# Optimization experiments

Measured on AMD Instinct MI355X. Metric: run time of the kernel, lower is better.

## Reference

```python
import jax, jax.numpy as jnp
import numpy as np

B, S, H = 2, 1024, 4096
NH, NKV, HD = 32, 8, 128
GROUPS = NH // NKV  # num_key_value_groups
ROPE_THETA = 10000.0


def setup_inputs() -> dict:
    key = jax.random.key(0)
    k0, k1, k2 = jax.random.split(key, 3)
    x = jax.random.normal(k0, (B, S, H), jnp.float32)
    w_qkv = jax.random.normal(k1, (H, (NH + 2 * NKV) * HD), jnp.float32) * (1.0 / np.sqrt(H))
    w_o = jax.random.normal(k2, (NH * HD, H), jnp.float32) * (1.0 / np.sqrt(H))
    # rotary cos/sin tables (llama freqs_cis, interleaved-pair convention)
    inv_freq = 1.0 / (ROPE_THETA ** (np.arange(0, HD, 2, dtype=np.float64) / HD))
    freqs = np.outer(np.arange(S, dtype=np.float64), inv_freq)  # [S, HD/2]
    cos = jnp.asarray(np.cos(freqs), jnp.float32)
    sin = jnp.asarray(np.sin(freqs), jnp.float32)
    # additive causal mask [1,1,S,S]
    causal = np.tril(np.ones((S, S), dtype=bool))
    mask = jnp.asarray(np.where(causal, 0.0, -1e9), jnp.float32)[None, None]
    return {"x": x, "w_qkv": w_qkv, "w_o": w_o, "cos": cos, "sin": sin, "mask": mask}


def _rope(t, cos, sin):
    # t: [B,S,N,HD]; rotate interleaved (even, odd) pairs like complex mult by freqs_cis
    t2 = t.reshape(t.shape[:-1] + (HD // 2, 2))
    t0, t1 = t2[..., 0], t2[..., 1]
    c = cos[None, :, None, :]  # [1,S,1,HD/2]
    s = sin[None, :, None, :]
    r0 = t0 * c - t1 * s
    r1 = t0 * s + t1 * c
    return jnp.stack([r0, r1], axis=-1).reshape(t.shape)


def reference(x, w_qkv, w_o, cos, sin, mask):
    b, s, _ = x.shape
    xqkv = (x @ w_qkv).reshape(b, s, NH + 2 * NKV, HD)
    xq = xqkv[:, :, :NH]                  # [b,s,NH,HD]
    xk = xqkv[:, :, NH:NH + NKV]          # [b,s,NKV,HD]
    xv = xqkv[:, :, NH + NKV:]            # [b,s,NKV,HD]
    xq = _rope(xq, cos, sin)
    xk = _rope(xk, cos, sin)
    # GQA: repeat kv heads to match query heads (repeat_interleave on head dim)
    k = jnp.repeat(xk, GROUPS, axis=2)
    v = jnp.repeat(xv, GROUPS, axis=2)
    scores = jnp.einsum('bqhd,bkhd->bhqk', xq, k) / np.float32(np.sqrt(HD))
    scores = scores + mask
    probs = jax.nn.softmax(scores.astype(jnp.float32), axis=-1).astype(xq.dtype)
    out = jnp.einsum('bhqk,bkhd->bqhd', probs, v).reshape(b, s, NH * HD)
    return out @ w_o
```

## Files before the change

### kernel.cpp

```cpp
#include <hip/hip_runtime.h>
#include <cstdint>
#include <cstddef>

typedef short bf16x8 __attribute__((ext_vector_type(8)));
typedef float f32x4 __attribute__((ext_vector_type(4)));

__device__ __forceinline__ unsigned short f2bf(float f) {
  unsigned int u = __builtin_bit_cast(unsigned int, f);
  u += 0x7fffu + ((u >> 16) & 1u);
  return (unsigned short)(u >> 16);
}

__global__ void k_convert(const float* __restrict__ in, unsigned short* __restrict__ out, int n4) {
  int i = blockIdx.x * blockDim.x + threadIdx.x;
  if (i >= n4) return;
  float4 v = ((const float4*)in)[i];
  ushort4 o;
  o.x = f2bf(v.x); o.y = f2bf(v.y); o.z = f2bf(v.z); o.w = f2bf(v.w);
  ((ushort4*)out)[i] = o;
}

__global__ __launch_bounds__(256) void k_transpose(const float* __restrict__ src,
                                                   unsigned short* __restrict__ dst,
                                                   int K, int N) {
  __shared__ float t[64][65];
  const int n0 = blockIdx.x * 64, k0 = blockIdx.y * 64;
  const int tid = threadIdx.x;
  const int lr = tid >> 4, lc = (tid & 15) * 4;
#pragma unroll
  for (int i = 0; i < 4; ++i) {
    float4 v = *(const float4*)(src + (size_t)(k0 + i * 16 + lr) * N + n0 + lc);
    t[i * 16 + lr][lc] = v.x;
    t[i * 16 + lr][lc + 1] = v.y;
    t[i * 16 + lr][lc + 2] = v.z;
    t[i * 16 + lr][lc + 3] = v.w;
  }
  __syncthreads();
  const int nr = tid >> 3, kk = (tid & 7) * 8;
#pragma unroll
  for (int i = 0; i < 2; ++i) {
    int n = nr + i * 32;
    bf16x8 v;
#pragma unroll
    for (int j = 0; j < 8; ++j) v[j] = (short)f2bf(t[kk + j][n]);
    *(bf16x8*)(dst + (size_t)(n0 + n) * K + k0 + kk) = v;
  }
}

template <int MODE>
__global__ __launch_bounds__(256) void k_gemm(const unsigned short* __restrict__ A,
                                              const unsigned short* __restrict__ Bt,
                                              float* __restrict__ C,
                                              unsigned short* __restrict__ Qr,
                                              unsigned short* __restrict__ Kr,
                                              unsigned short* __restrict__ Vt,
                                              const float* __restrict__ cosT,
                                              const float* __restrict__ sinT,
                                              int M, int N, int K) {
  __shared__ __align__(16) unsigned short lA[128 * 64];
  __shared__ __align__(16) unsigned short lB[128 * 64];
  const int tid = threadIdx.x;
  const int lane = tid & 63, wv = tid >> 6;
  const int wr = wv >> 1, wc = wv & 1;
  const int lid = blockIdx.y * gridDim.x + blockIdx.x;
  const int cpx = (gridDim.x * gridDim.y) >> 3;
  const int swz = (lid & 7) * cpx + (lid >> 3);
  const int bm = (swz % gridDim.x) * 128, bn = (swz / gridDim.x) * 128;
  const int l16 = lane & 15, lhi = lane >> 4;
  f32x4 acc[4][4] = {};
  bf16x8 ar[4], br[4];

#pragma unroll
  for (int i = 0; i < 4; ++i) {
    int c = tid + i * 256, row = c >> 3, c16 = c & 7;
    ar[i] = *(const bf16x8*)(A + (size_t)(bm + row) * K + 0 + c16 * 8);
    br[i] = *(const bf16x8*)(Bt + (size_t)(bn + row) * K + 0 + c16 * 8);
  }
  const int nkt = K >> 6;
  for (int kt = 0; kt < nkt; ++kt) {
    __syncthreads();
#pragma unroll
    for (int i = 0; i < 4; ++i) {
      int c = tid + i * 256, row = c >> 3, c16 = c & 7;
      int pc = c16 ^ (row & 7);
      *(bf16x8*)((char*)lA + row * 128 + pc * 16) = ar[i];
      *(bf16x8*)((char*)lB + row * 128 + pc * 16) = br[i];
    }
    __syncthreads();
    if (kt + 1 < nkt) {
      int kofs = (kt + 1) << 6;
#pragma unroll
      for (int i = 0; i < 4; ++i) {
        int c = tid + i * 256, row = c >> 3, c16 = c & 7;
        ar[i] = *(const bf16x8*)(A + (size_t)(bm + row) * K + kofs + c16 * 8);
        br[i] = *(const bf16x8*)(Bt + (size_t)(bn + row) * K + kofs + c16 * 8);
      }
    }
#pragma unroll
    for (int s = 0; s < 2; ++s) {
      bf16x8 af[4], bfr[4];
#pragma unroll
      for (int f = 0; f < 4; ++f) {
        int rowa = wr * 64 + f * 16 + l16;
        int ca = (s * 4 + lhi) ^ (rowa & 7);
        af[f] = *(const bf16x8*)((char*)lA + rowa * 128 + ca * 16);
        int rowb = wc * 64 + f * 16 + l16;
        int cb = (s * 4 + lhi) ^ (rowb & 7);
        bfr[f] = *(const bf16x8*)((char*)lB + rowb * 128 + cb * 16);
      }
#pragma unroll
      for (int fi = 0; fi < 4; ++fi)
#pragma unroll
        for (int fj = 0; fj < 4; ++fj)
          acc[fi][fj] = __builtin_amdgcn_mfma_f32_16x16x32_bf16(af[fi], bfr[fj], acc[fi][fj], 0, 0, 0);
    }
  }

  if (MODE == 0) {
#pragma unroll
    for (int fi = 0; fi < 4; ++fi) {
      int rbase = bm + wr * 64 + fi * 16 + lhi * 4;
#pragma unroll
      for (int fj = 0; fj < 4; ++fj) {
        int col = bn + wc * 64 + fj * 16 + l16;
#pragma unroll
        for (int r = 0; r < 4; ++r)
          C[(size_t)(rbase + r) * N + col] = acc[fi][fj][r];
      }
    }
  } else {
#pragma unroll
    for (int fi = 0; fi < 4; ++fi) {
      int rbase = bm + wr * 64 + fi * 16 + lhi * 4;
      int b = rbase >> 10, sbase = rbase & 1023;
#pragma unroll
      for (int fj = 0; fj < 4; ++fj) {
        int col = bn + wc * 64 + fj * 16 + l16;
        if (col < 5120) {
          int i = (col & 127) >> 1;
          float sgn = (col & 1) ? 1.0f : -1.0f;
          unsigned short* dst;
          if (col < 4096)
            dst = Qr + ((size_t)(b * 32 + (col >> 7)) * 1024) * 128 + (col & 127);
          else
            dst = Kr + ((size_t)(b * 8 + ((col - 4096) >> 7)) * 1024) * 128 + (col & 127);
#pragma unroll
          for (int r = 0; r < 4; ++r) {
            float own = acc[fi][fj][r];
            float other = __shfl_xor(own, 1);
            int s = sbase + r;
            float c = cosT[s * 64 + i], sn = sinT[s * 64 + i];
            dst[(size_t)s * 128] = f2bf(own * c + sgn * other * sn);
          }
        } else {
          int kvh = (col - 5120) >> 7, d = col & 127;
          unsigned short* dst = Vt + ((size_t)(b * 8 + kvh) * 128 + d) * 1024;
#pragma unroll
          for (int r = 0; r < 4; ++r) dst[sbase + r] = f2bf(acc[fi][fj][r]);
        }
      }
    }
  }
}

__global__ __launch_bounds__(256) void k_attn(const unsigned short* __restrict__ Qr,
                                              const unsigned short* __restrict__ Kr,
                                              const unsigned short* __restrict__ Vt,
                                              unsigned short* __restrict__ Out) {
  __shared__ __align__(16) unsigned short lK[64 * 128];
  __shared__ __align__(16) unsigned short lV[128 * 64];
  __shared__ __align__(16) unsigned short lP[4 * 16 * 64];
  const int tid = threadIdx.x, lane = tid & 63, wv = tid >> 6;
  const int qt = blockIdx.x, h = blockIdx.y, b = blockIdx.z;
  const int kvh = h >> 2;
  const int q0 = qt * 64;
  const int l16 = lane & 15, lhi = lane >> 4;

  const unsigned short* Qbase = Qr + ((size_t)(b * 32 + h) * 1024 + q0 + wv * 16 + l16) * 128;
  bf16x8 qf[4];
#pragma unroll
  for (int s = 0; s < 4; ++s) qf[s] = *(const bf16x8*)(Qbase + s * 32 + lhi * 8);

  const unsigned short* Kbase = Kr + (size_t)(b * 8 + kvh) * 1024 * 128;
  const unsigned short* Vbase = Vt + (size_t)(b * 8 + kvh) * 128 * 1024;

  f32x4 oacc[8] = {};
  float mrow[4] = {-1e30f, -1e30f, -1e30f, -1e30f};
  float lrow[4] = {0.f, 0.f, 0.f, 0.f};
  const int ntk = qt + 1;
  bf16x8 kreg[4], vreg[4];

#pragma unroll
  for (int i = 0; i < 4; ++i) {
    int c = tid + i * 256;
    int krow = c >> 4, kc = c & 15;
    kreg[i] = *(const bf16x8*)(Kbase + (size_t)krow * 128 + kc * 8);
    int vrow = c >> 3, vc = c & 7;
    vreg[i] = *(const bf16x8*)(Vbase + (size_t)vrow * 1024 + vc * 8);
  }

  for (int kt = 0; kt < ntk; ++kt) {
    const int k0 = kt * 64;
    __syncthreads();
#pragma unroll
    for (int i = 0; i < 4; ++i) {
      int c = tid + i * 256;
      int krow = c >> 4, kc = c & 15;
      *(bf16x8*)((char*)lK + krow * 256 + (kc ^ (krow & 7)) * 16) = kreg[i];
      int vrow = c >> 3, vc = c & 7;
      *(bf16x8*)((char*)lV + vrow * 128 + (vc ^ (vrow & 7)) * 16) = vreg[i];
    }
    __syncthreads();

    if (kt + 1 < ntk) {
      const int kn = (kt + 1) * 64;
#pragma unroll
      for (int i = 0; i < 4; ++i) {
        int c = tid + i * 256;
        int krow = c >> 4, kc = c & 15;
        kreg[i] = *(const bf16x8*)(Kbase + (size_t)(kn + krow) * 128 + kc * 8);
        int vrow = c >> 3, vc = c & 7;
        vreg[i] = *(const bf16x8*)(Vbase + (size_t)vrow * 1024 + kn + vc * 8);
      }
    }

    f32x4 sacc[4] = {};
#pragma unroll
    for (int kf = 0; kf < 4; ++kf) {
      int rowk = kf * 16 + l16;
#pragma unroll
      for (int s = 0; s < 4; ++s) {
        int ck = (s * 4 + lhi) ^ (rowk & 7);
        bf16x8 kfr = *(const bf16x8*)((char*)lK + rowk * 256 + ck * 16);
        sacc[kf] = __builtin_amdgcn_mfma_f32_16x16x32_bf16(qf[s], kfr, sacc[kf], 0, 0, 0);
      }
    }

    const int qg = q0 + wv * 16 + lhi * 4;
    float mt[4] = {-1e30f, -1e30f, -1e30f, -1e30f};
#pragma unroll
    for (int kf = 0; kf < 4; ++kf) {
      int kg = k0 + kf * 16 + l16;
#pragma unroll
      for (int r = 0; r < 4; ++r) {
        float v = sacc[kf][r] * 0.08838834764831845f;
        v = (kg <= qg + r) ? v : -1e9f;
        sacc[kf][r] = v;
        mt[r] = fmaxf(mt[r], v);
      }
    }
#pragma unroll
    for (int r = 0; r < 4; ++r) {
#pragma unroll
      for (int off = 1; off < 16; off <<= 1) mt[r] = fmaxf(mt[r], __shfl_xor(mt[r], off));
    }
    float alpha[4], rs[4];
#pragma unroll
    for (int r = 0; r < 4; ++r) {
      float mn = fmaxf(mrow[r], mt[r]);
      alpha[r] = __expf(mrow[r] - mn);
      mrow[r] = mn;
      rs[r] = 0.f;
    }
#pragma unroll
    for (int kf = 0; kf < 4; ++kf) {
      int key = kf * 16 + l16;
#pragma unroll
      for (int r = 0; r < 4; ++r) {
        float p = __expf(sacc[kf][r] - mrow[r]);
        rs[r] += p;
        int prow = lhi * 4 + r;
        int addr = wv * 2048 + ((prow * 128 + key * 2) ^ ((prow & 7) << 4));
        *(unsigned short*)((char*)lP + addr) = f2bf(p);
      }
    }
#pragma unroll
    for (int r = 0; r < 4; ++r) {
#pragma unroll
      for (int off = 1; off < 16; off <<= 1) rs[r] += __shfl_xor(rs[r], off);
      lrow[r] = lrow[r] * alpha[r] + rs[r];
    }
#pragma unroll
    for (int nf = 0; nf < 8; ++nf)
#pragma unroll
      for (int r = 0; r < 4; ++r) oacc[nf][r] *= alpha[r];

#pragma unroll
    for (int s2 = 0; s2 < 2; ++s2) {
      int prow = l16;
      int paddr = wv * 2048 + ((prow * 128 + s2 * 64 + lhi * 16) ^ ((prow & 7) << 4));
      bf16x8 pa = *(const bf16x8*)((char*)lP + paddr);
#pragma unroll
      for (int nf = 0; nf < 8; ++nf) {
        int rowd = nf * 16 + l16;
        int cv = (s2 * 4 + lhi) ^ (rowd & 7);
        bf16x8 vfr = *(const bf16x8*)((char*)lV + rowd * 128 + cv * 16);
        oacc[nf] = __builtin_amdgcn_mfma_f32_16x16x32_bf16(pa, vfr, oacc[nf], 0, 0, 0);
      }
    }
  }

  unsigned short* Ob = Out + ((size_t)(b * 1024) + q0 + wv * 16 + lhi * 4) * 4096 + h * 128;
#pragma unroll
  for (int r = 0; r < 4; ++r) {
    float inv = 1.f / lrow[r];
#pragma unroll
    for (int nf = 0; nf < 8; ++nf)
      Ob[(size_t)r * 4096 + nf * 16 + l16] = f2bf(oacc[nf][r] * inv);
  }
}

extern "C" void kernel_launch(void* const* d_in, const int* in_sizes, int n_in,
                              void* d_out, int out_size, void* d_ws, size_t ws_size,
                              hipStream_t stream) {
  const float* x = (const float*)d_in[0];
  const float* w_qkv = (const float*)d_in[1];
  const float* w_o = (const float*)d_in[2];
  const float* cosT = (const float*)d_in[3];
  const float* sinT = (const float*)d_in[4];

  char* ws = (char*)d_ws;
  unsigned short* wqkv_t = (unsigned short*)(ws);
  unsigned short* wo_t   = (unsigned short*)(ws + 50331648);
  unsigned short* xb     = (unsigned short*)(ws + 83886080);
  unsigned short* Qr     = (unsigned short*)(ws + 100663296);
  unsigned short* Kr     = (unsigned short*)(ws + 117440512);
  unsigned short* Vt     = (unsigned short*)(ws + 121634816);
  unsigned short* attn   = (unsigned short*)(ws + 125829120);

  k_convert<<<8192, 256, 0, stream>>>(x, xb, 2048 * 4096 / 4);
  k_transpose<<<dim3(6144 / 64, 4096 / 64), 256, 0, stream>>>(w_qkv, wqkv_t, 4096, 6144);
  k_transpose<<<dim3(4096 / 64, 4096 / 64), 256, 0, stream>>>(w_o, wo_t, 4096, 4096);
  k_gemm<1><<<dim3(16, 48), 256, 0, stream>>>(xb, wqkv_t, nullptr, Qr, Kr, Vt, cosT, sinT,
                                              2048, 6144, 4096);
  k_attn<<<dim3(16, 32, 2), 256, 0, stream>>>(Qr, Kr, Vt, attn);
  k_gemm<0><<<dim3(16, 32), 256, 0, stream>>>(attn, wo_t, (float*)d_out, nullptr, nullptr, nullptr,
                                              nullptr, nullptr, 2048, 4096, 4096);
}
```

Baseline: 329.2 us.

## Replace QKV GEMM with 256x256 tiled 8-phase pipelined kernel using direct-to-LDS loads

Adds a new QKV projection GEMM with 256x256 output tiles, 512 threads and a double-buffered LDS. Tiles are staged with global_load_lds direct-to-LDS copies, interleaved across eight compute phases with explicit vmcnt waits, barriers and setprio. The goal is more data reuse per tile and overlap of global loads with MFMA work, in place of the 128x128 register-staged GEMM. The fused RoPE/V-transpose epilogue is kept, and the output GEMM becomes a non-template kernel. This adds hand-tuned waitcnt logic that must line up exactly with the load counts, and the 192-block grid may leave some compute units idle.

```diff
diff --git a/kernel.cpp b/kernel.cpp
--- a/kernel.cpp
+++ b/kernel.cpp
@@ -9,6 +9,12 @@
   unsigned int u = __builtin_bit_cast(unsigned int, f);
   u += 0x7fffu + ((u >> 16) & 1u);
   return (unsigned short)(u >> 16);
+}
+
+__device__ __forceinline__ void gload_lds(const unsigned short* g, unsigned short* l) {
+  __builtin_amdgcn_global_load_lds(
+      (const __attribute__((address_space(1))) unsigned int*)g,
+      (__attribute__((address_space(3))) unsigned int*)l, 16, 0, 0);
 }
 
 __global__ void k_convert(const float* __restrict__ in, unsigned short* __restrict__ out, int n4) {
@@ -47,16 +53,131 @@
   }
 }
 
-template <int MODE>
+__global__ __launch_bounds__(512, 2) void k_gemm8p(const unsigned short* __restrict__ A,
+                                                   const unsigned short* __restrict__ Bt,
+                                                   unsigned short* __restrict__ Qr,
+                                                   unsigned short* __restrict__ Kr,
+                                                   unsigned short* __restrict__ Vt,
+                                                   const float* __restrict__ cosT,
+                                                   const float* __restrict__ sinT) {
+  __shared__ __align__(16) unsigned short lds[2][2][2][128 * 64];
+  const int tid = threadIdx.x;
+  const int lane = tid & 63, wv = tid >> 6;
+  const int wr = wv >> 2, wc = wv & 3;
+  const int l16 = lane & 15, lhi = lane >> 4;
+  const int lid = blockIdx.x;
+  const int swz = (lid & 7) * 24 + (lid >> 3);
+  const int bm2 = (swz & 7) * 256, bn2 = (swz >> 3) * 256;
+
+  f32x4 acc[8][4] = {};
+
+  auto STAGE = [&](int buf, int mat, int half, const unsigned short* srcM, int srcRowBase, int kt) {
+#pragma unroll
+    for (int j = 0; j < 2; ++j) {
+      int row = j * 64 + wv * 8 + (lane >> 3);
+      int chunk = (lane & 7) ^ (row & 7);
+      gload_lds(srcM + (size_t)(srcRowBase + row) * 4096 + kt * 64 + chunk * 8,
+                &lds[buf][mat][half][(j * 512 + wv * 64) * 8]);
+    }
+  };
+
+  auto PHASE = [&](int buf, int mh, int nh, int stg, int b2, int m2, int h2,
+                   const unsigned short* s2, int rb2, int kt2, int vm) {
+    bf16x8 af[4][2], bfr[2][2];
+#pragma unroll
+    for (int fl = 0; fl < 4; ++fl) {
+      int ra = fl * 32 + wr * 16 + l16;
+#pragma unroll
+      for (int s = 0; s < 2; ++s)
+        af[fl][s] = *(const bf16x8*)&lds[buf][0][mh][ra * 64 + (((s * 4 + lhi) ^ (ra & 7)) * 8)];
+    }
+#pragma unroll
+    for (int fl = 0; fl < 2; ++fl) {
+      int rb = fl * 64 + wc * 16 + l16;
+#pragma unroll
+      for (int s = 0; s < 2; ++s)
+        bfr[fl][s] = *(const bf16x8*)&lds[buf][1][nh][rb * 64 + (((s * 4 + lhi) ^ (rb & 7)) * 8)];
+    }
+    if (stg) STAGE(b2, m2, h2, s2, rb2, kt2);
+    __builtin_amdgcn_s_barrier();
+    __builtin_amdgcn_s_setprio(1);
+#pragma unroll
+    for (int fl = 0; fl < 4; ++fl)
+#pragma unroll
+      for (int gl = 0; gl < 2; ++gl)
+#pragma unroll
+        for (int s = 0; s < 2; ++s)
+          acc[mh * 4 + fl][nh * 2 + gl] =
+              __builtin_amdgcn_mfma_f32_16x16x32_bf16(af[fl][s], bfr[gl][s],
+                                                      acc[mh * 4 + fl][nh * 2 + gl], 0, 0, 0);
+    __builtin_amdgcn_s_setprio(0);
+    if (vm == 4) {
+      asm volatile("s_waitcnt vmcnt(4)" ::: "memory");
+      __builtin_amdgcn_sched_barrier(0);
+    } else if (vm == 0) {
+      asm volatile("s_waitcnt vmcnt(0)" ::: "memory");
+      __builtin_amdgcn_sched_barrier(0);
+    }
+    __builtin_amdgcn_s_barrier();
+  };
+
+  STAGE(0, 0, 0, A, bm2, 0);       STAGE(0, 0, 1, A, bm2 + 128, 0);
+  STAGE(0, 1, 0, Bt, bn2, 0);      STAGE(0, 1, 1, Bt, bn2 + 128, 0);
+  STAGE(1, 0, 0, A, bm2, 1);       STAGE(1, 0, 1, A, bm2 + 128, 1);
+  STAGE(1, 1, 0, Bt, bn2, 1);      STAGE(1, 1, 1, Bt, bn2 + 128, 1);
+  asm volatile("s_waitcnt vmcnt(8)" ::: "memory");
+  __builtin_amdgcn_sched_barrier(0);
+  __builtin_amdgcn_s_barrier();
+
+  for (int i = 0; i < 32; ++i) {
+    const int t1 = 2 * i + 1, t2 = 2 * i + 2, t3 = 2 * i + 3;
+    const int nf = (i > 0), nl = (i < 31);
+    PHASE(0, 0, 0, nf, 1, 0, 0, A, bm2, t1, -1);
+    PHASE(0, 1, 0, nf, 1, 1, 1, Bt, bn2 + 128, t1, -1);
+    PHASE(0, 1, 1, nl, 0, 1, 0, Bt, bn2, t2, -1);
+    PHASE(0, 0, 1, nl, 0, 0, 1, A, bm2 + 128, t2, nl ? 4 : 0);
+    PHASE(1, 0, 0, nl, 0, 0, 0, A, bm2, t2, -1);
+    PHASE(1, 1, 0, nl, 0, 1, 1, Bt, bn2 + 128, t2, -1);
+    PHASE(1, 1, 1, nl, 1, 1, 0, Bt, bn2, t3, -1);
+    PHASE(1, 0, 1, nl, 1, 0, 1, A, bm2 + 128, t3, nl ? 4 : -1);
+  }
+
+#pragma unroll
+  for (int fi = 0; fi < 8; ++fi) {
+    int rbase = bm2 + fi * 32 + wr * 16 + lhi * 4;
+    int b = rbase >> 10, sbase = rbase & 1023;
+#pragma unroll
+    for (int fj = 0; fj < 4; ++fj) {
+      int col = bn2 + fj * 64 + wc * 16 + l16;
+      if (col < 5120) {
+        int ip = (col & 127) >> 1;
+        float sgn = (col & 1) ? 1.0f : -1.0f;
+        unsigned short* dst;
+        if (col < 4096)
+          dst = Qr + ((size_t)(b * 32 + (col >> 7)) * 1024) * 128 + (col & 127);
+        else
+          dst = Kr + ((size_t)(b * 8 + ((col - 4096) >> 7)) * 1024) * 128 + (col & 127);
+#pragma unroll
+        for (int r = 0; r < 4; ++r) {
+          float own = acc[fi][fj][r];
+          float other = __shfl_xor(own, 1);
+          int s = sbase + r;
+          float c = cosT[s * 64 + ip], sn = sinT[s * 64 + ip];
+          dst[(size_t)s * 128] = f2bf(own * c + sgn * other * sn);
+        }
+      } else {
+        int kvh = (col - 5120) >> 7, d = col & 127;
+        unsigned short* dst = Vt + ((size_t)(b * 8 + kvh) * 128 + d) * 1024;
+#pragma unroll
+        for (int r = 0; r < 4; ++r) dst[sbase + r] = f2bf(acc[fi][fj][r]);
+      }
+    }
+  }
+}
+
 __global__ __launch_bounds__(256) void k_gemm(const unsigned short* __restrict__ A,
                                               const unsigned short* __restrict__ Bt,
-                                              float* __restrict__ C,
-                                              unsigned short* __restrict__ Qr,
-                                              unsigned short* __restrict__ Kr,
-                                              unsigned short* __restrict__ Vt,
-                                              const float* __restrict__ cosT,
-                                              const float* __restrict__ sinT,
-                                              int M, int N, int K) {
+                                              float* __restrict__ C, int M, int N, int K) {
   __shared__ __align__(16) unsigned short lA[128 * 64];
   __shared__ __align__(16) unsigned short lB[128 * 64];
   const int tid = threadIdx.x;
@@ -115,50 +236,15 @@
           acc[fi][fj] = __builtin_amdgcn_mfma_f32_16x16x32_bf16(af[fi], bfr[fj], acc[fi][fj], 0, 0, 0);
     }
   }
-
-  if (MODE == 0) {
-#pragma unroll
-    for (int fi = 0; fi < 4; ++fi) {
-      int rbase = bm + wr * 64 + fi * 16 + lhi * 4;
-#pragma unroll
-      for (int fj = 0; fj < 4; ++fj) {
-        int col = bn + wc * 64 + fj * 16 + l16;
-#pragma unroll
-        for (int r = 0; r < 4; ++r)
-          C[(size_t)(rbase + r) * N + col] = acc[fi][fj][r];
-      }
-    }
-  } else {
-#pragma unroll
-    for (int fi = 0; fi < 4; ++fi) {
-      int rbase = bm + wr * 64 + fi * 16 + lhi * 4;
-      int b = rbase >> 10, sbase = rbase & 1023;
-#pragma unroll
-      for (int fj = 0; fj < 4; ++fj) {
-        int col = bn + wc * 64 + fj * 16 + l16;
-        if (col < 5120) {
-          int i = (col & 127) >> 1;
-          float sgn = (col & 1) ? 1.0f : -1.0f;
-          unsigned short* dst;
-          if (col < 4096)
-            dst = Qr + ((size_t)(b * 32 + (col >> 7)) * 1024) * 128 + (col & 127);
-          else
-            dst = Kr + ((size_t)(b * 8 + ((col - 4096) >> 7)) * 1024) * 128 + (col & 127);
-#pragma unroll
-          for (int r = 0; r < 4; ++r) {
-            float own = acc[fi][fj][r];
-            float other = __shfl_xor(own, 1);
-            int s = sbase + r;
-            float c = cosT[s * 64 + i], sn = sinT[s * 64 + i];
-            dst[(size_t)s * 128] = f2bf(own * c + sgn * other * sn);
-          }
-        } else {
-          int kvh = (col - 5120) >> 7, d = col & 127;
-          unsigned short* dst = Vt + ((size_t)(b * 8 + kvh) * 128 + d) * 1024;
-#pragma unroll
-          for (int r = 0; r < 4; ++r) dst[sbase + r] = f2bf(acc[fi][fj][r]);
-        }
-      }
+#pragma unroll
+  for (int fi = 0; fi < 4; ++fi) {
+    int rbase = bm + wr * 64 + fi * 16 + lhi * 4;
+#pragma unroll
+    for (int fj = 0; fj < 4; ++fj) {
+      int col = bn + wc * 64 + fj * 16 + l16;
+#pragma unroll
+      for (int r = 0; r < 4; ++r)
+        C[(size_t)(rbase + r) * N + col] = acc[fi][fj][r];
     }
   }
 }
@@ -331,9 +417,7 @@
   k_convert<<<8192, 256, 0, stream>>>(x, xb, 2048 * 4096 / 4);
   k_transpose<<<dim3(6144 / 64, 4096 / 64), 256, 0, stream>>>(w_qkv, wqkv_t, 4096, 6144);
   k_transpose<<<dim3(4096 / 64, 4096 / 64), 256, 0, stream>>>(w_o, wo_t, 4096, 4096);
-  k_gemm<1><<<dim3(16, 48), 256, 0, stream>>>(xb, wqkv_t, nullptr, Qr, Kr, Vt, cosT, sinT,
-                                              2048, 6144, 4096);
+  k_gemm8p<<<192, 512, 0, stream>>>(xb, wqkv_t, Qr, Kr, Vt, cosT, sinT);
   k_attn<<<dim3(16, 32, 2), 256, 0, stream>>>(Qr, Kr, Vt, attn);
-  k_gemm<0><<<dim3(16, 32), 256, 0, stream>>>(attn, wo_t, (float*)d_out, nullptr, nullptr, nullptr,
-                                              nullptr, nullptr, 2048, 4096, 4096);
-}
+  k_gemm<<<dim3(16, 32), 256, 0, stream>>>(attn, wo_t, (float*)d_out, 2048, 4096, 4096);
+}
```

Measured after the change: 347.8 us. +5.7%, slower.

## Double attention query tile per block and merge prep kernels into one launch

Applied to the files above, without the earlier changes.

The attention kernel now handles 128 queries per block, with each wave covering two 16-row query groups. Each K/V tile loaded into LDS therefore feeds twice as many MFMAs, which halves K/V global traffic and staging per query. The cost is more registers (launch bounds set to 2 blocks per SIMD), half as many blocks, and more causal-diagonal waste since the last two key tiles are partly masked. Separately, the bf16 conversion of x and the two weight transposes are fused into one launch to remove launch overhead.

```diff
diff --git a/kernel.cpp b/kernel.cpp
--- a/kernel.cpp
+++ b/kernel.cpp
@@ -11,21 +11,10 @@
   return (unsigned short)(u >> 16);
 }
 
-__global__ void k_convert(const float* __restrict__ in, unsigned short* __restrict__ out, int n4) {
-  int i = blockIdx.x * blockDim.x + threadIdx.x;
-  if (i >= n4) return;
-  float4 v = ((const float4*)in)[i];
-  ushort4 o;
-  o.x = f2bf(v.x); o.y = f2bf(v.y); o.z = f2bf(v.z); o.w = f2bf(v.w);
-  ((ushort4*)out)[i] = o;
-}
-
-__global__ __launch_bounds__(256) void k_transpose(const float* __restrict__ src,
-                                                   unsigned short* __restrict__ dst,
-                                                   int K, int N) {
+__device__ __forceinline__ void transpose_tile(const float* __restrict__ src,
+                                               unsigned short* __restrict__ dst,
+                                               int K, int N, int n0, int k0, int tid) {
   __shared__ float t[64][65];
-  const int n0 = blockIdx.x * 64, k0 = blockIdx.y * 64;
-  const int tid = threadIdx.x;
   const int lr = tid >> 4, lc = (tid & 15) * 4;
 #pragma unroll
   for (int i = 0; i < 4; ++i) {
@@ -44,6 +33,28 @@
 #pragma unroll
     for (int j = 0; j < 8; ++j) v[j] = (short)f2bf(t[kk + j][n]);
     *(bf16x8*)(dst + (size_t)(n0 + n) * K + k0 + kk) = v;
+  }
+}
+
+__global__ __launch_bounds__(256) void k_prep(const float* __restrict__ x,
+                                              const float* __restrict__ w_qkv,
+                                              const float* __restrict__ w_o,
+                                              unsigned short* __restrict__ xb,
+                                              unsigned short* __restrict__ wqkv_t,
+                                              unsigned short* __restrict__ wo_t) {
+  const int bid = blockIdx.x, tid = threadIdx.x;
+  if (bid < 8192) {
+    int i = bid * 256 + tid;
+    float4 v = ((const float4*)x)[i];
+    ushort4 o;
+    o.x = f2bf(v.x); o.y = f2bf(v.y); o.z = f2bf(v.z); o.w = f2bf(v.w);
+    ((ushort4*)xb)[i] = o;
+  } else if (bid < 14336) {
+    int t = bid - 8192;
+    transpose_tile(w_qkv, wqkv_t, 4096, 6144, (t % 96) * 64, (t / 96) * 64, tid);
+  } else {
+    int t = bid - 14336;
+    transpose_tile(w_o, wo_t, 4096, 4096, (t & 63) * 64, (t >> 6) * 64, tid);
   }
 }
 
@@ -163,31 +174,38 @@
   }
 }
 
-__global__ __launch_bounds__(256) void k_attn(const unsigned short* __restrict__ Qr,
-                                              const unsigned short* __restrict__ Kr,
-                                              const unsigned short* __restrict__ Vt,
-                                              unsigned short* __restrict__ Out) {
+__global__ __launch_bounds__(256, 2) void k_attn(const unsigned short* __restrict__ Qr,
+                                                 const unsigned short* __restrict__ Kr,
+                                                 const unsigned short* __restrict__ Vt,
+                                                 unsigned short* __restrict__ Out) {
   __shared__ __align__(16) unsigned short lK[64 * 128];
   __shared__ __align__(16) unsigned short lV[128 * 64];
-  __shared__ __align__(16) unsigned short lP[4 * 16 * 64];
+  __shared__ __align__(16) unsigned short lP[4 * 32 * 64];
   const int tid = threadIdx.x, lane = tid & 63, wv = tid >> 6;
-  const int qt = blockIdx.x, h = blockIdx.y, b = blockIdx.z;
+  const int qtb = blockIdx.x, h = blockIdx.y, b = blockIdx.z;
   const int kvh = h >> 2;
-  const int q0 = qt * 64;
+  const int q0 = qtb * 128;
   const int l16 = lane & 15, lhi = lane >> 4;
 
-  const unsigned short* Qbase = Qr + ((size_t)(b * 32 + h) * 1024 + q0 + wv * 16 + l16) * 128;
-  bf16x8 qf[4];
-#pragma unroll
-  for (int s = 0; s < 4; ++s) qf[s] = *(const bf16x8*)(Qbase + s * 32 + lhi * 8);
+  bf16x8 qf[2][4];
+#pragma unroll
+  for (int g = 0; g < 2; ++g) {
+    const unsigned short* Qb =
+        Qr + ((size_t)(b * 32 + h) * 1024 + q0 + wv * 32 + g * 16 + l16) * 128;
+#pragma unroll
+    for (int s = 0; s < 4; ++s) qf[g][s] = *(const bf16x8*)(Qb + s * 32 + lhi * 8);
+  }
 
   const unsigned short* Kbase = Kr + (size_t)(b * 8 + kvh) * 1024 * 128;
   const unsigned short* Vbase = Vt + (size_t)(b * 8 + kvh) * 128 * 1024;
 
-  f32x4 oacc[8] = {};
-  float mrow[4] = {-1e30f, -1e30f, -1e30f, -1e30f};
-  float lrow[4] = {0.f, 0.f, 0.f, 0.f};
-  const int ntk = qt + 1;
+  f32x4 oacc[2][8] = {};
+  float mrow[2][4], lrow[2][4];
+#pragma unroll
+  for (int g = 0; g < 2; ++g)
+#pragma unroll
+    for (int r = 0; r < 4; ++r) { mrow[g][r] = -1e30f; lrow[g][r] = 0.f; }
+  const int ntk = 2 * qtb + 2;
   bf16x8 kreg[4], vreg[4];
 
 #pragma unroll
@@ -224,7 +242,7 @@
       }
     }
 
-    f32x4 sacc[4] = {};
+    f32x4 sacc[2][4] = {};
 #pragma unroll
     for (int kf = 0; kf < 4; ++kf) {
       int rowk = kf * 16 + l16;
@@ -232,81 +250,95 @@
       for (int s = 0; s < 4; ++s) {
         int ck = (s * 4 + lhi) ^ (rowk & 7);
         bf16x8 kfr = *(const bf16x8*)((char*)lK + rowk * 256 + ck * 16);
-        sacc[kf] = __builtin_amdgcn_mfma_f32_16x16x32_bf16(qf[s], kfr, sacc[kf], 0, 0, 0);
-      }
-    }
-
-    const int qg = q0 + wv * 16 + lhi * 4;
-    float mt[4] = {-1e30f, -1e30f, -1e30f, -1e30f};
-#pragma unroll
-    for (int kf = 0; kf < 4; ++kf) {
-      int kg = k0 + kf * 16 + l16;
+        sacc[0][kf] = __builtin_amdgcn_mfma_f32_16x16x32_bf16(qf[0][s], kfr, sacc[0][kf], 0, 0, 0);
+        sacc[1][kf] = __builtin_amdgcn_mfma_f32_16x16x32_bf16(qf[1][s], kfr, sacc[1][kf], 0, 0, 0);
+      }
+    }
+
+    float alpha[2][4];
+#pragma unroll
+    for (int g = 0; g < 2; ++g) {
+      const int qg = q0 + wv * 32 + g * 16 + lhi * 4;
+      float mt[4] = {-1e30f, -1e30f, -1e30f, -1e30f};
+#pragma unroll
+      for (int kf = 0; kf < 4; ++kf) {
+        int kg = k0 + kf * 16 + l16;
+#pragma unroll
+        for (int r = 0; r < 4; ++r) {
+          float v = sacc[g][kf][r] * 0.08838834764831845f;
+          v = (kg <= qg + r) ? v : -1e9f;
+          sacc[g][kf][r] = v;
+          mt[r] = fmaxf(mt[r], v);
+        }
+      }
 #pragma unroll
       for (int r = 0; r < 4; ++r) {
-        float v = sacc[kf][r] * 0.08838834764831845f;
-        v = (kg <= qg + r) ? v : -1e9f;
-        sacc[kf][r] = v;
-        mt[r] = fmaxf(mt[r], v);
-      }
-    }
-#pragma unroll
-    for (int r = 0; r < 4; ++r) {
-#pragma unroll
-      for (int off = 1; off < 16; off <<= 1) mt[r] = fmaxf(mt[r], __shfl_xor(mt[r], off));
-    }
-    float alpha[4], rs[4];
-#pragma unroll
-    for (int r = 0; r < 4; ++r) {
-      float mn = fmaxf(mrow[r], mt[r]);
-      alpha[r] = __expf(mrow[r] - mn);
-      mrow[r] = mn;
-      rs[r] = 0.f;
-    }
-#pragma unroll
-    for (int kf = 0; kf < 4; ++kf) {
-      int key = kf * 16 + l16;
+#pragma unroll
+        for (int off = 1; off < 16; off <<= 1) mt[r] = fmaxf(mt[r], __shfl_xor(mt[r], off));
+      }
+      float rs[4];
 #pragma unroll
       for (int r = 0; r < 4; ++r) {
-        float p = __expf(sacc[kf][r] - mrow[r]);
-        rs[r] += p;
-        int prow = lhi * 4 + r;
-        int addr = wv * 2048 + ((prow * 128 + key * 2) ^ ((prow & 7) << 4));
-        *(unsigned short*)((char*)lP + addr) = f2bf(p);
-      }
-    }
-#pragma unroll
-    for (int r = 0; r < 4; ++r) {
-#pragma unroll
-      for (int off = 1; off < 16; off <<= 1) rs[r] += __shfl_xor(rs[r], off);
-      lrow[r] = lrow[r] * alpha[r] + rs[r];
-    }
-#pragma unroll
-    for (int nf = 0; nf < 8; ++nf)
-#pragma unroll
-      for (int r = 0; r < 4; ++r) oacc[nf][r] *= alpha[r];
+        float mn = fmaxf(mrow[g][r], mt[r]);
+        alpha[g][r] = __expf(mrow[g][r] - mn);
+        mrow[g][r] = mn;
+        rs[r] = 0.f;
+      }
+#pragma unroll
+      for (int kf = 0; kf < 4; ++kf) {
+        int key = kf * 16 + l16;
+#pragma unroll
+        for (int r = 0; r < 4; ++r) {
+          float p = __expf(sacc[g][kf][r] - mrow[g][r]);
+          rs[r] += p;
+          int prow = g * 16 + lhi * 4 + r;
+          int addr = wv * 4096 + ((prow * 128 + key * 2) ^ ((prow & 7) << 4));
+          *(unsigned short*)((char*)lP + addr) = f2bf(p);
+        }
+      }
+#pragma unroll
+      for (int r = 0; r < 4; ++r) {
+#pragma unroll
+        for (int off = 1; off < 16; off <<= 1) rs[r] += __shfl_xor(rs[r], off);
+        lrow[g][r] = lrow[g][r] * alpha[g][r] + rs[r];
+      }
+#pragma unroll
+      for (int nf = 0; nf < 8; ++nf)
+#pragma unroll
+        for (int r = 0; r < 4; ++r) oacc[g][nf][r] *= alpha[g][r];
+    }
 
 #pragma unroll
     for (int s2 = 0; s2 < 2; ++s2) {
-      int prow = l16;
-      int paddr = wv * 2048 + ((prow * 128 + s2 * 64 + lhi * 16) ^ ((prow & 7) << 4));
-      bf16x8 pa = *(const bf16x8*)((char*)lP + paddr);
+      bf16x8 pa[2];
+#pragma unroll
+      for (int g = 0; g < 2; ++g) {
+        int prow = g * 16 + l16;
+        int paddr = wv * 4096 + ((prow * 128 + s2 * 64 + lhi * 16) ^ ((prow & 7) << 4));
+        pa[g] = *(const bf16x8*)((char*)lP + paddr);
+      }
 #pragma unroll
       for (int nf = 0; nf < 8; ++nf) {
         int rowd = nf * 16 + l16;
         int cv = (s2 * 4 + lhi) ^ (rowd & 7);
         bf16x8 vfr = *(const bf16x8*)((char*)lV + rowd * 128 + cv * 16);
-        oacc[nf] = __builtin_amdgcn_mfma_f32_16x16x32_bf16(pa, vfr, oacc[nf], 0, 0, 0);
-      }
-    }
-  }
-
-  unsigned short* Ob = Out + ((size_t)(b * 1024) + q0 + wv * 16 + lhi * 4) * 4096 + h * 128;
-#pragma unroll
-  for (int r = 0; r < 4; ++r) {
-    float inv = 1.f / lrow[r];
-#pragma unroll
-    for (int nf = 0; nf < 8; ++nf)
-      Ob[(size_t)r * 4096 + nf * 16 + l16] = f2bf(oacc[nf][r] * inv);
+        oacc[0][nf] = __builtin_amdgcn_mfma_f32_16x16x32_bf16(pa[0], vfr, oacc[0][nf], 0, 0, 0);
+        oacc[1][nf] = __builtin_amdgcn_mfma_f32_16x16x32_bf16(pa[1], vfr, oacc[1][nf], 0, 0, 0);
+      }
+    }
+  }
+
+#pragma unroll
+  for (int g = 0; g < 2; ++g) {
+    unsigned short* Ob =
+        Out + ((size_t)(b * 1024) + q0 + wv * 32 + g * 16 + lhi * 4) * 4096 + h * 128;
+#pragma unroll
+    for (int r = 0; r < 4; ++r) {
+      float inv = 1.f / lrow[g][r];
+#pragma unroll
+      for (int nf = 0; nf < 8; ++nf)
+        Ob[(size_t)r * 4096 + nf * 16 + l16] = f2bf(oacc[g][nf][r] * inv);
+    }
   }
 }
 
@@ -328,12 +360,10 @@
   unsigned short* Vt     = (unsigned short*)(ws + 121634816);
   unsigned short* attn   = (unsigned short*)(ws + 125829120);
 
-  k_convert<<<8192, 256, 0, stream>>>(x, xb, 2048 * 4096 / 4);
-  k_transpose<<<dim3(6144 / 64, 4096 / 64), 256, 0, stream>>>(w_qkv, wqkv_t, 4096, 6144);
-  k_transpose<<<dim3(4096 / 64, 4096 / 64), 256, 0, stream>>>(w_o, wo_t, 4096, 4096);
+  k_prep<<<18432, 256, 0, stream>>>(x, w_qkv, w_o, xb, wqkv_t, wo_t);
   k_gemm<1><<<dim3(16, 48), 256, 0, stream>>>(xb, wqkv_t, nullptr, Qr, Kr, Vt, cosT, sinT,
                                               2048, 6144, 4096);
-  k_attn<<<dim3(16, 32, 2), 256, 0, stream>>>(Qr, Kr, Vt, attn);
+  k_attn<<<dim3(8, 32, 2), 256, 0, stream>>>(Qr, Kr, Vt, attn);
   k_gemm<0><<<dim3(16, 32), 256, 0, stream>>>(attn, wo_t, (float*)d_out, nullptr, nullptr, nullptr,
                                               nullptr, nullptr, 2048, 4096, 4096);
 }
```

Measured after the change: 333.6 us. No clear change (+1.4%).
